# Kernel optimization log

Hardware: AMD Instinct MI355X
Metric: run time of the kernel (lower is better)

Reference implementation:

```python
import jax, jax.numpy as jnp
import numpy as np
import math

B, S, D, H, FF = 2, 2048, 1024, 16, 4096
E = D // H  # per-head dim = 64
LN_EPS = 1e-5


def _layernorm(x, g, b):
    m = jnp.mean(x, axis=-1, keepdims=True)
    v = jnp.var(x, axis=-1, keepdims=True)
    return (x - m) * jax.lax.rsqrt(v + LN_EPS) * g + b


def setup_inputs() -> dict:
    key = jax.random.key(0)
    ks = jax.random.split(key, 12)
    std = 0.02
    return {
        "inputs": jax.random.normal(ks[0], (B, S, D), dtype=jnp.float32),
        "ln1_g": jnp.ones((D,), jnp.float32),
        "ln1_b": jnp.zeros((D,), jnp.float32),
        # per-head q/k/v Linear(D, E) stacked along head axis: [H, D, E]
        "wq": jax.random.normal(ks[1], (H, D, E), jnp.float32) * std,
        "bq": jax.random.normal(ks[2], (H, E), jnp.float32) * std,
        "wk": jax.random.normal(ks[3], (H, D, E), jnp.float32) * std,
        "bk": jax.random.normal(ks[4], (H, E), jnp.float32) * std,
        "wv": jax.random.normal(ks[5], (H, D, E), jnp.float32) * std,
        "bv": jax.random.normal(ks[6], (H, E), jnp.float32) * std,
        "wo": jax.random.normal(ks[7], (D, D), jnp.float32) * std,
        "bo": jnp.zeros((D,), jnp.float32),
        "ln2_g": jnp.ones((D,), jnp.float32),
        "ln2_b": jnp.zeros((D,), jnp.float32),
        "w1": jax.random.normal(ks[8], (D, FF), jnp.float32) * std,
        "b1": jnp.zeros((FF,), jnp.float32),
        "w2": jax.random.normal(ks[9], (FF, D), jnp.float32) * std,
        "b2": jnp.zeros((D,), jnp.float32),
    }


def reference(inputs, ln1_g, ln1_b, wq, bq, wk, bk, wv, bv, wo, bo,
              ln2_g, ln2_b, w1, b1, w2, b2):
    d_model = inputs.shape[-1]
    scale = jnp.asarray(math.sqrt(d_model), inputs.dtype)  # NOTE: sqrt(d_model), not d_head

    x1 = _layernorm(inputs, ln1_g, ln1_b)
    # batched per-head projections (original uses H separate Linear layers)
    q = jnp.einsum('bsd,hde->bhse', x1, wq) + bq[None, :, None, :]
    k = jnp.einsum('bsd,hde->bhse', x1, wk) + bk[None, :, None, :]
    v = jnp.einsum('bsd,hde->bhse', x1, wv) + bv[None, :, None, :]

    scores = jnp.einsum('bhqe,bhke->bhqk', q, k) / scale
    # original: nn.Softmax(dim=1) on [B, S_q, S_k] -> softmax over the QUERY axis
    attn = jax.nn.softmax(scores, axis=2)
    a = jnp.einsum('bhqk,bhke->bhqe', attn, v)  # [B, H, S, E]

    # concat heads along feature dim (head 0 first)
    bsz, _, slen, _ = a.shape
    a = a.transpose(0, 2, 1, 3).reshape(bsz, slen, d_model)
    msa = a @ wo + bo

    inter = msa + inputs
    x2 = _layernorm(inter, ln2_g, ln2_b)
    mlp = jax.nn.gelu(x2 @ w1 + b1, approximate=False) @ w2 + b2
    return mlp + inter
```

## Files before the change

kernel.cpp:

```cpp
#include <hip/hip_runtime.h>
#include <hip/hip_bf16.h>

typedef unsigned short u16;
typedef __attribute__((ext_vector_type(8))) short short8;
typedef __attribute__((ext_vector_type(4))) float f32x4;
typedef __attribute__((ext_vector_type(4))) unsigned short us4;
typedef __attribute__((ext_vector_type(4))) float float4v;

#define DEV __device__ __forceinline__

DEV float b2f(u16 v){ return __uint_as_float(((unsigned)v)<<16); }
DEV u16 f2b(float f){
  unsigned u = __float_as_uint(f);
  u = u + 0x7FFFu + ((u>>16)&1u);
  return (u16)(u>>16);
}
DEV f32x4 mfma16(short8 a, short8 b, f32x4 c){
  return __builtin_amdgcn_mfma_f32_16x16x32_bf16(a, b, c, 0, 0, 0);
}
DEV void async16(const void* g, const void* l){
  __builtin_amdgcn_global_load_lds(
    (const __attribute__((address_space(1))) unsigned int*)(uintptr_t)g,
    (__attribute__((address_space(3))) unsigned int*)(unsigned int)(uintptr_t)l,
    16, 0, 0);
}

__global__ __launch_bounds__(256) void ln_k(const float* __restrict__ xin,
    const float* __restrict__ g, const float* __restrict__ bb, u16* __restrict__ y)
{
  const int row = blockIdx.x, t = threadIdx.x, l = t&63, w = t>>6;
  const float4v rr = *(const float4v*)(xin + (size_t)row*1024 + t*4);
  float v[4] = {rr[0], rr[1], rr[2], rr[3]};
  float s  = v[0]+v[1]+v[2]+v[3];
  float ss = v[0]*v[0]+v[1]*v[1]+v[2]*v[2]+v[3]*v[3];
#pragma unroll
  for (int off=32; off>=1; off>>=1){
    s  += __shfl_down(s,  off, 64);
    ss += __shfl_down(ss, off, 64);
  }
  __shared__ float rs[4], rq[4];
  if (l==0){ rs[w]=s; rq[w]=ss; }
  __syncthreads();
  const float S = rs[0]+rs[1]+rs[2]+rs[3];
  const float Q = rq[0]+rq[1]+rq[2]+rq[3];
  const float mean = S*(1.0f/1024.0f);
  const float var  = Q*(1.0f/1024.0f) - mean*mean;
  const float rstd = rsqrtf(var + 1e-5f);
  const float4v gg = *(const float4v*)(g  + t*4);
  const float4v bv = *(const float4v*)(bb + t*4);
  us4 o;
#pragma unroll
  for (int j=0;j<4;j++) o[j] = f2b((v[j]-mean)*rstd*gg[j] + bv[j]);
  *(us4*)(y + (size_t)row*1024 + t*4) = o;
}

__global__ void transpose_k(const float* __restrict__ src, u16* __restrict__ dst,
                            int ldsrc, int lddst)
{
  __shared__ u16 tile[32][33];
  const int tx = threadIdx.x & 31, ty = threadIdx.x >> 5;
  const int c0 = blockIdx.x*32, r0 = blockIdx.y*32;
#pragma unroll
  for (int i=0;i<32;i+=8) tile[ty+i][tx] = f2b(src[(size_t)(r0+ty+i)*ldsrc + c0+tx]);
  __syncthreads();
#pragma unroll
  for (int i=0;i<32;i+=8) dst[(size_t)(c0+ty+i)*lddst + r0+tx] = tile[tx][ty+i];
}

__global__ void pack_qkv_k(const float* __restrict__ wq, const float* __restrict__ wk,
                           const float* __restrict__ wv, u16* __restrict__ BT)
{
  __shared__ u16 tile[32][33];
  const int z = blockIdx.z, which = z>>4, h = z&15;
  const float* w = (which==0?wq:(which==1?wk:wv)) + (size_t)h*1024*64;
  u16* d = BT + (size_t)(which*1024 + h*64)*1024;
  const int tx = threadIdx.x & 31, ty = threadIdx.x >> 5;
  const int c0 = blockIdx.x*32, r0 = blockIdx.y*32;
#pragma unroll
  for (int i=0;i<32;i+=8) tile[ty+i][tx] = f2b(w[(size_t)(r0+ty+i)*64 + c0+tx]);
  __syncthreads();
#pragma unroll
  for (int i=0;i<32;i+=8) d[(size_t)(c0+ty+i)*1024 + r0+tx] = tile[tx][ty+i];
}

__global__ void pack_bias_k(const float* __restrict__ bq, const float* __restrict__ bk,
                            const float* __restrict__ bv, float* __restrict__ dst)
{
  const int t = blockIdx.x*256 + threadIdx.x;
  const float* s = (t < 1024) ? bq : (t < 2048 ? bk : bv);
  dst[t] = s[t & 1023];
}

template<int EPI>
__global__ __launch_bounds__(256) void gemm_bt(
    const u16* __restrict__ A, const u16* __restrict__ BT,
    const float* __restrict__ bias, const float* __restrict__ resf,
    u16* __restrict__ outb, float* __restrict__ outf,
    int K, int lda, int ldb, int ldc)
{
  __shared__ u16 Asm[128*32];
  __shared__ u16 Bsm[128*32];
  const int t = threadIdx.x, l = t&63, w = t>>6;
  const int bn = blockIdx.x, bm = blockIdx.y;
  const u16* gA = A  + (size_t)(bm*128 + (t>>2))*lda + (t&3)*8;
  const u16* gB = BT + (size_t)(bn*128 + (t>>2))*ldb + (t&3)*8;
  char* lA = (char*)Asm + t*16;
  char* lB = (char*)Bsm + t*16;
  const int wr = (w>>1)*64, wc = (w&1)*64;
  f32x4 acc[4][4] = {};
  for (int kt = 0; kt < K; kt += 32) {
    __syncthreads();
    async16(gA + kt,                    lA);
    async16(gA + kt + (size_t)64*lda,   lA + 4096);
    async16(gB + kt,                    lB);
    async16(gB + kt + (size_t)64*ldb,   lB + 4096);
    __syncthreads();
    short8 af[4], bf[4];
#pragma unroll
    for (int m=0;m<4;m++) af[m] = *(const short8*)&Asm[(wr + m*16 + (l&15))*32 + (l>>4)*8];
#pragma unroll
    for (int n=0;n<4;n++) bf[n] = *(const short8*)&Bsm[(wc + n*16 + (l&15))*32 + (l>>4)*8];
#pragma unroll
    for (int m=0;m<4;m++)
#pragma unroll
      for (int n=0;n<4;n++)
        acc[m][n] = mfma16(af[m], bf[n], acc[m][n]);
  }
  const int rowb = bm*128 + wr, colb = bn*128 + wc;
#pragma unroll
  for (int m=0;m<4;m++)
#pragma unroll
    for (int n=0;n<4;n++){
      const int col = colb + n*16 + (l&15);
      const float bv = bias[col];
#pragma unroll
      for (int j=0;j<4;j++){
        const int row = rowb + m*16 + (l>>4)*4 + j;
        float v = acc[m][n][j] + bv;
        const size_t idx = (size_t)row*ldc + col;
        if constexpr (EPI==0)      outb[idx] = f2b(v);
        else if constexpr (EPI==1) outf[idx] = v + resf[idx];
        else                       outb[idx] = f2b(0.5f*v*(1.0f + erff(v*0.70710678118654752f)));
      }
    }
}

template<int EPI>
__global__ __launch_bounds__(256) void gemm_bt64(
    const u16* __restrict__ A, const u16* __restrict__ BT,
    const float* __restrict__ bias, const float* __restrict__ resf,
    u16* __restrict__ outb, float* __restrict__ outf,
    int K, int lda, int ldb, int ldc)
{
  __shared__ u16 Asm[128*32];
  __shared__ u16 Bsm[64*32];
  const int t = threadIdx.x, l = t&63, w = t>>6;
  const int bn = blockIdx.x, bm = blockIdx.y;
  const u16* gA = A  + (size_t)(bm*128 + (t>>2))*lda + (t&3)*8;
  const u16* gB = BT + (size_t)(bn*64  + (t>>2))*ldb + (t&3)*8;
  char* lA = (char*)Asm + t*16;
  char* lB = (char*)Bsm + t*16;
  const int wr = w*32;
  f32x4 acc[2][4] = {};
  for (int kt = 0; kt < K; kt += 32) {
    __syncthreads();
    async16(gA + kt,                    lA);
    async16(gA + kt + (size_t)64*lda,   lA + 4096);
    async16(gB + kt,                    lB);
    __syncthreads();
    short8 af[2], bf[4];
#pragma unroll
    for (int m=0;m<2;m++) af[m] = *(const short8*)&Asm[(wr + m*16 + (l&15))*32 + (l>>4)*8];
#pragma unroll
    for (int n=0;n<4;n++) bf[n] = *(const short8*)&Bsm[(n*16 + (l&15))*32 + (l>>4)*8];
#pragma unroll
    for (int m=0;m<2;m++)
#pragma unroll
      for (int n=0;n<4;n++)
        acc[m][n] = mfma16(af[m], bf[n], acc[m][n]);
  }
  const int rowb = bm*128 + wr, colb = bn*64;
#pragma unroll
  for (int m=0;m<2;m++)
#pragma unroll
    for (int n=0;n<4;n++){
      const int col = colb + n*16 + (l&15);
      const float bv = bias[col];
#pragma unroll
      for (int j=0;j<4;j++){
        const int row = rowb + m*16 + (l>>4)*4 + j;
        float v = acc[m][n][j] + bv;
        const size_t idx = (size_t)row*ldc + col;
        if constexpr (EPI==0)      outb[idx] = f2b(v);
        else if constexpr (EPI==1) outf[idx] = v + resf[idx];
        else                       outb[idx] = f2b(0.5f*v*(1.0f + erff(v*0.70710678118654752f)));
      }
    }
}


__global__ __launch_bounds__(256) void attn_stats(const u16* __restrict__ QKV, float* __restrict__ L)
{
  const int g = blockIdx.x;
  const int xcd = g & 7, s_ = g >> 3;
  const int bh   = xcd*4 + (s_ & 3);
  const int kblk = (s_ >> 2) & 15;
  const int part = s_ >> 6;
  const int b = bh>>4, h = bh&15;
  const u16* Qb = QKV + (size_t)b*2048*3072 + h*64;
  const u16* Kb = Qb + 1024;
  __shared__ u16 Klds[128*64];
  __shared__ float red[4][128];
  const int t = threadIdx.x, l = t&63, w = t>>6;
#pragma unroll
  for (int i=0;i<8;i++){
    const int c = t + i*256, r = c>>4, ch = c&15;
    us4 v = *(const us4*)(Kb + (size_t)(kblk*128 + r)*3072 + ch*4);
    *(us4*)((char*)Klds + ((r*128 + ch*8) ^ ((r&7)<<4))) = v;
  }
  __syncthreads();
  short8 kf[8][2];
#pragma unroll
  for (int n=0;n<8;n++){
    const int r = n*16 + (l&15);
    const int sw = (r&7)<<4;
#pragma unroll
    for (int ks=0;ks<2;ks++)
      kf[n][ks] = *(const short8*)((char*)Klds + ((r*128 + ks*64 + (l>>4)*16) ^ sw));
  }
  float Lacc[8] = {0,0,0,0,0,0,0,0};
  for (int qt = part*8; qt < part*8 + 8; qt++){
    const int qb = qt*128 + w*32;
    short8 qf[2][2];
#pragma unroll
    for (int m=0;m<2;m++)
#pragma unroll
      for (int ks=0;ks<2;ks++)
        qf[m][ks] = *(const short8*)(Qb + (size_t)(qb + m*16 + (l&15))*3072 + ks*32 + (l>>4)*8);
#pragma unroll
    for (int m=0;m<2;m++)
#pragma unroll
      for (int n=0;n<8;n++){
        f32x4 s = {};
        s = mfma16(qf[m][0], kf[n][0], s);
        s = mfma16(qf[m][1], kf[n][1], s);
#pragma unroll
        for (int j=0;j<4;j++) Lacc[n] += __expf(s[j]*0.03125f);
      }
  }
#pragma unroll
  for (int n=0;n<8;n++){
    Lacc[n] += __shfl_xor(Lacc[n], 16, 64);
    Lacc[n] += __shfl_xor(Lacc[n], 32, 64);
  }
  if (l < 16){
#pragma unroll
    for (int n=0;n<8;n++) red[w][n*16 + l] = Lacc[n];
  }
  __syncthreads();
  if (t < 128)
    L[(size_t)part*65536 + (size_t)bh*2048 + kblk*128 + t]
        = red[0][t]+red[1][t]+red[2][t]+red[3][t];
}

__global__ __launch_bounds__(256) void attn_pv(const u16* __restrict__ QKV,
    const float* __restrict__ L, u16* __restrict__ Aout)
{
  const int g = blockIdx.x;
  const int xcd = g & 7, s_ = g >> 3;
  const int bh = xcd*4 + (s_ & 3);
  const int qblk = s_ >> 2;
  const int b = bh>>4, h = bh&15;
  const u16* Qb = QKV + (size_t)b*2048*3072 + h*64;
  const u16* Kb = Qb + 1024;
  const u16* Vb = Qb + 2048;
  const float* L0 = L + (size_t)bh*2048;
  const float* L1 = L0 + 65536;
  __shared__ u16 Klds[64*64];
  __shared__ u16 VT[64*66];
  __shared__ u16 P[64*68];
  __shared__ float invL[64];
  const int t = threadIdx.x, l = t&63, w = t>>6;
  short8 qf[2];
#pragma unroll
  for (int ks=0;ks<2;ks++)
    qf[ks] = *(const short8*)(Qb + (size_t)(qblk*64 + w*16 + (l&15))*3072 + ks*32 + (l>>4)*8);
  f32x4 acc[4] = {};
  for (int kt=0; kt<2048; kt+=64){
    __syncthreads();
#pragma unroll
    for (int i=0;i<4;i++){
      const int c = t + i*256, r = c>>4, ch = c&15;
      us4 kv = *(const us4*)(Kb + (size_t)(kt + r)*3072 + ch*4);
      *(us4*)((char*)Klds + ((r*128 + ch*8) ^ ((r&7)<<4))) = kv;
      us4 vv = *(const us4*)(Vb + (size_t)(kt + r)*3072 + ch*4);
#pragma unroll
      for (int jj=0;jj<4;jj++) VT[(ch*4+jj)*66 + r] = vv[jj];
    }
    if (t < 64) invL[t] = 1.0f / (L0[kt + t] + L1[kt + t]);
    __syncthreads();
    float il[4];
#pragma unroll
    for (int n=0;n<4;n++) il[n] = invL[n*16 + (l&15)];
#pragma unroll
    for (int n=0;n<4;n++){
      const int r = n*16 + (l&15);
      const int sw = (r&7)<<4;
      const short8 kf0 = *(const short8*)((char*)Klds + ((r*128 +      (l>>4)*16) ^ sw));
      const short8 kf1 = *(const short8*)((char*)Klds + ((r*128 + 64 + (l>>4)*16) ^ sw));
      f32x4 s = {};
      s = mfma16(qf[0], kf0, s);
      s = mfma16(qf[1], kf1, s);
      const int prow = w*16 + (l>>4)*4;
      const int pcol = n*16 + (l&15);
#pragma unroll
      for (int j=0;j<4;j++)
        P[(prow+j)*68 + pcol] = f2b(__expf(s[j]*0.03125f) * il[n]);
    }
    __syncthreads();
#pragma unroll
    for (int kk=0;kk<2;kk++){
      const short8 af = *(const short8*)&P[(w*16 + (l&15))*68 + kk*32 + (l>>4)*8];
#pragma unroll
      for (int n=0;n<4;n++){
        const short8 bf = *(const short8*)&VT[(n*16 + (l&15))*66 + kk*32 + (l>>4)*8];
        acc[n] = mfma16(af, bf, acc[n]);
      }
    }
  }
  const int rowb = b*2048 + qblk*64 + w*16;
  const int colb = h*64;
#pragma unroll
  for (int n=0;n<4;n++)
#pragma unroll
    for (int j=0;j<4;j++){
      const int row = rowb + (l>>4)*4 + j;
      const int col = colb + n*16 + (l&15);
      Aout[(size_t)row*1024 + col] = f2b(acc[n][j]);
    }
}

extern "C" void kernel_launch(void* const* d_in, const int* in_sizes, int n_in,
                              void* d_out, int out_size, void* d_ws, size_t ws_size,
                              hipStream_t stream)
{
  const float* x    = (const float*)d_in[0];
  const float* ln1g = (const float*)d_in[1];
  const float* ln1b = (const float*)d_in[2];
  const float* wq   = (const float*)d_in[3];
  const float* bq   = (const float*)d_in[4];
  const float* wk   = (const float*)d_in[5];
  const float* bk   = (const float*)d_in[6];
  const float* wv   = (const float*)d_in[7];
  const float* bv   = (const float*)d_in[8];
  const float* wo   = (const float*)d_in[9];
  const float* bo   = (const float*)d_in[10];
  const float* ln2g = (const float*)d_in[11];
  const float* ln2b = (const float*)d_in[12];
  const float* w1   = (const float*)d_in[13];
  const float* b1   = (const float*)d_in[14];
  const float* w2   = (const float*)d_in[15];
  const float* b2   = (const float*)d_in[16];
  float* out = (float*)d_out;

  char* ws = (char*)d_ws;
  u16*   x1      = (u16*)  (ws + 0);
  u16*   QKV     = (u16*)  (ws + 8388608);
  u16*   H1      = (u16*)  (ws + 8388608);
  float* Lbuf    = (float*)(ws + 41943040);
  u16*   Aout    = (u16*)  (ws + 42467328);
  u16*   packbuf = (u16*)  (ws + 50855936);
  float* inter   = (float*)(ws + 59244544);
  float* biasqkv = (float*)(ws + 76021760);
  u16*   x2 = x1;

  pack_bias_k<<<12, 256, 0, stream>>>(bq, bk, bv, biasqkv);

  ln_k<<<4096, 256, 0, stream>>>(x, ln1g, ln1b, x1);
  pack_qkv_k<<<dim3(2,32,48), 256, 0, stream>>>(wq, wk, wv, packbuf);
  gemm_bt<0><<<dim3(24,32), 256, 0, stream>>>(x1, packbuf, biasqkv,
      nullptr, QKV, nullptr, 1024, 1024, 1024, 3072);

  attn_stats<<<1024, 256, 0, stream>>>(QKV, Lbuf);
  attn_pv  <<<1024, 256, 0, stream>>>(QKV, Lbuf, Aout);

  transpose_k<<<dim3(32,32), 256, 0, stream>>>(wo, packbuf, 1024, 1024);
  gemm_bt64<1><<<dim3(16,32), 256, 0, stream>>>(Aout, packbuf, bo,
      x, nullptr, inter, 1024, 1024, 1024, 1024);

  ln_k<<<4096, 256, 0, stream>>>(inter, ln2g, ln2b, x2);

  transpose_k<<<dim3(128,32), 256, 0, stream>>>(w1, packbuf, 4096, 1024);
  gemm_bt<2><<<dim3(32,32), 256, 0, stream>>>(x2, packbuf, b1,
      nullptr, H1, nullptr, 1024, 1024, 1024, 4096);

  transpose_k<<<dim3(32,128), 256, 0, stream>>>(w2, packbuf, 1024, 4096);
  gemm_bt64<1><<<dim3(16,32), 256, 0, stream>>>(H1, packbuf, b2,
      inter, nullptr, out, 4096, 4096, 4096, 1024);
}
```

Baseline: 478.9 us.

## Prefetch K/V tiles and Q fragments into registers in attention kernels

attn_pv now loads the next K/V tile and its inverse-normalizer into registers while the current tile is computed, then writes them to LDS at the top of the next iteration, which removes one barrier per iteration. attn_stats double-buffers its Q fragments in registers so the next query tile's loads overlap the current MFMA/exp work. A new small inv_l kernel precomputes reciprocal column sums once instead of each attn_pv block recomputing them. The cost is higher register pressure from the prefetch buffers and one extra kernel launch.

```diff
diff --git a/kernel.cpp b/kernel.cpp
--- a/kernel.cpp
+++ b/kernel.cpp
@@ -91,6 +91,12 @@
   dst[t] = s[t & 1023];
 }
 
+__global__ __launch_bounds__(256) void inv_l(const float* __restrict__ L, float* __restrict__ invL)
+{
+  const int i = blockIdx.x*256 + threadIdx.x;
+  invL[i] = 1.0f / (L[i] + L[i + 65536]);
+}
+
 template<int EPI>
 __global__ __launch_bounds__(256) void gemm_bt(
     const u16* __restrict__ A, const u16* __restrict__ BT,
@@ -229,14 +235,24 @@
       kf[n][ks] = *(const short8*)((char*)Klds + ((r*128 + ks*64 + (l>>4)*16) ^ sw));
   }
   float Lacc[8] = {0,0,0,0,0,0,0,0};
-  for (int qt = part*8; qt < part*8 + 8; qt++){
-    const int qb = qt*128 + w*32;
-    short8 qf[2][2];
+  short8 qf[2][2], qn[2][2];
+  {
+    const int qb = part*1024 + w*32;
 #pragma unroll
     for (int m=0;m<2;m++)
 #pragma unroll
       for (int ks=0;ks<2;ks++)
         qf[m][ks] = *(const short8*)(Qb + (size_t)(qb + m*16 + (l&15))*3072 + ks*32 + (l>>4)*8);
+  }
+  for (int qt = 0; qt < 8; qt++){
+    if (qt < 7){
+      const int qb = part*1024 + (qt+1)*128 + w*32;
+#pragma unroll
+      for (int m=0;m<2;m++)
+#pragma unroll
+        for (int ks=0;ks<2;ks++)
+          qn[m][ks] = *(const short8*)(Qb + (size_t)(qb + m*16 + (l&15))*3072 + ks*32 + (l>>4)*8);
+    }
 #pragma unroll
     for (int m=0;m<2;m++)
 #pragma unroll
@@ -247,6 +263,12 @@
 #pragma unroll
         for (int j=0;j<4;j++) Lacc[n] += __expf(s[j]*0.03125f);
       }
+    if (qt < 7){
+#pragma unroll
+      for (int m=0;m<2;m++)
+#pragma unroll
+        for (int ks=0;ks<2;ks++) qf[m][ks] = qn[m][ks];
+    }
   }
 #pragma unroll
   for (int n=0;n<8;n++){
@@ -264,7 +286,7 @@
 }
 
 __global__ __launch_bounds__(256) void attn_pv(const u16* __restrict__ QKV,
-    const float* __restrict__ L, u16* __restrict__ Aout)
+    const float* __restrict__ invL, u16* __restrict__ Aout)
 {
   const int g = blockIdx.x;
   const int xcd = g & 7, s_ = g >> 3;
@@ -274,34 +296,51 @@
   const u16* Qb = QKV + (size_t)b*2048*3072 + h*64;
   const u16* Kb = Qb + 1024;
   const u16* Vb = Qb + 2048;
-  const float* L0 = L + (size_t)bh*2048;
-  const float* L1 = L0 + 65536;
+  const float* iL = invL + (size_t)bh*2048;
   __shared__ u16 Klds[64*64];
   __shared__ u16 VT[64*66];
   __shared__ u16 P[64*68];
-  __shared__ float invL[64];
+  __shared__ float iLs[64];
   const int t = threadIdx.x, l = t&63, w = t>>6;
   short8 qf[2];
 #pragma unroll
   for (int ks=0;ks<2;ks++)
     qf[ks] = *(const short8*)(Qb + (size_t)(qblk*64 + w*16 + (l&15))*3072 + ks*32 + (l>>4)*8);
+  int rr[4], cc[4];
+#pragma unroll
+  for (int i=0;i<4;i++){ const int c = t + i*256; rr[i] = c>>4; cc[i] = c&15; }
+  us4 kreg[4], vreg[4];
+#pragma unroll
+  for (int i=0;i<4;i++){
+    kreg[i] = *(const us4*)(Kb + (size_t)rr[i]*3072 + cc[i]*4);
+    vreg[i] = *(const us4*)(Vb + (size_t)rr[i]*3072 + cc[i]*4);
+  }
+  float ilreg = (t < 64) ? iL[t] : 0.0f;
   f32x4 acc[4] = {};
   for (int kt=0; kt<2048; kt+=64){
+#pragma unroll
+    for (int i=0;i<4;i++)
+      *(us4*)((char*)Klds + ((rr[i]*128 + cc[i]*8) ^ ((rr[i]&7)<<4))) = kreg[i];
+    if (t < 64) iLs[t] = ilreg;
     __syncthreads();
 #pragma unroll
     for (int i=0;i<4;i++){
-      const int c = t + i*256, r = c>>4, ch = c&15;
-      us4 kv = *(const us4*)(Kb + (size_t)(kt + r)*3072 + ch*4);
-      *(us4*)((char*)Klds + ((r*128 + ch*8) ^ ((r&7)<<4))) = kv;
-      us4 vv = *(const us4*)(Vb + (size_t)(kt + r)*3072 + ch*4);
-#pragma unroll
-      for (int jj=0;jj<4;jj++) VT[(ch*4+jj)*66 + r] = vv[jj];
-    }
-    if (t < 64) invL[t] = 1.0f / (L0[kt + t] + L1[kt + t]);
-    __syncthreads();
+#pragma unroll
+      for (int jj=0;jj<4;jj++) VT[(cc[i]*4+jj)*66 + rr[i]] = vreg[i][jj];
+    }
+    if (kt + 64 < 2048){
+      const u16* Kn = Kb + (size_t)(kt+64)*3072;
+      const u16* Vn = Vb + (size_t)(kt+64)*3072;
+#pragma unroll
+      for (int i=0;i<4;i++){
+        kreg[i] = *(const us4*)(Kn + (size_t)rr[i]*3072 + cc[i]*4);
+        vreg[i] = *(const us4*)(Vn + (size_t)rr[i]*3072 + cc[i]*4);
+      }
+      if (t < 64) ilreg = iL[kt + 64 + t];
+    }
     float il[4];
 #pragma unroll
-    for (int n=0;n<4;n++) il[n] = invL[n*16 + (l&15)];
+    for (int n=0;n<4;n++) il[n] = iLs[n*16 + (l&15)];
 #pragma unroll
     for (int n=0;n<4;n++){
       const int r = n*16 + (l&15);
@@ -372,6 +411,7 @@
   u16*   packbuf = (u16*)  (ws + 50855936);
   float* inter   = (float*)(ws + 59244544);
   float* biasqkv = (float*)(ws + 76021760);
+  float* invLb   = (float*)(ws + 76038144);
   u16*   x2 = x1;
 
   pack_bias_k<<<12, 256, 0, stream>>>(bq, bk, bv, biasqkv);
@@ -382,7 +422,8 @@
       nullptr, QKV, nullptr, 1024, 1024, 1024, 3072);
 
   attn_stats<<<1024, 256, 0, stream>>>(QKV, Lbuf);
-  attn_pv  <<<1024, 256, 0, stream>>>(QKV, Lbuf, Aout);
+  inv_l<<<256, 256, 0, stream>>>(Lbuf, invLb);
+  attn_pv  <<<1024, 256, 0, stream>>>(QKV, invLb, Aout);
 
   transpose_k<<<dim3(32,32), 256, 0, stream>>>(wo, packbuf, 1024, 1024);
   gemm_bt64<1><<<dim3(16,32), 256, 0, stream>>>(Aout, packbuf, bo,
```

Result: no change. 476.9 us (-0.4%).
